# Kernel optimization log

Hardware: AMD Instinct MI355X
Metric: run time of the kernel (lower is better)

## Reference

```python
import jax, jax.numpy as jnp
import numpy as np

EPSILON = 0.1


def setup_inputs() -> dict:
    key = jax.random.key(0)
    ks = jax.random.split(key, 6)
    N, E, F_IN, F_OUT, NF = 50000, 800000, 256, 96, 3
    x = jax.random.normal(ks[0], (N, F_IN), dtype=jnp.float32)
    adj_vals = jax.random.uniform(ks[1], (E,), dtype=jnp.float32)
    d_scales = jax.random.uniform(ks[2], (NF, N), dtype=jnp.float32)
    # xavier-uniform-ish weights
    limit = np.sqrt(6.0 / (F_IN + F_OUT)).astype(np.float32)
    weights = jax.random.uniform(ks[3], (NF, F_IN, F_OUT), dtype=jnp.float32,
                                 minval=-limit, maxval=limit)
    bias = jnp.zeros((F_OUT,), dtype=jnp.float32)
    edge_index = jax.random.randint(ks[4], (2, E), 0, N, dtype=jnp.int32)
    return {"x": x, "adj_vals": adj_vals, "d_scales": d_scales,
            "weights": weights, "bias": bias, "edge_index": edge_index}


def reference(x, adj_vals, d_scales, weights, bias, edge_index):
    N = x.shape[0]
    row, col = edge_index[0], edge_index[1]

    # degree with self loops (add_remaining_self_loops adds 1 per node)
    deg = jax.ops.segment_sum(jnp.ones_like(adj_vals), row, num_segments=N) + 1.0
    eps_deg_inv = EPSILON / deg  # [N], diagonal of sparse_degree(..., epsilon)

    def spmm(t):  # symadj @ t via edge list
        return jax.ops.segment_sum(adj_vals[:, None] * t[col], row, num_segments=N)

    out = jnp.zeros((N, weights.shape[2]), dtype=x.dtype)
    n_filters = weights.shape[0]
    for ii in range(n_filters):
        sign = -1.0 if ii == 0 else 1.0  # Ad = symadj -/+ eps*diag(deg^-1)
        t = d_scales[ii][:, None] * (x @ weights[ii])          # D @ (x W)
        t = spmm(t) + sign * eps_deg_inv[:, None] * t          # Ad @ t
        t = d_scales[ii][:, None] * jax.nn.relu(t)             # D @ relu(t)
        out = out + t
    return out + bias
```

## Files before the change

### kernel.cpp

```cpp
#include <hip/hip_runtime.h>

#define EPSILON 0.1f
#define F_IN 256
#define F_OUT 96
#define NF 3
#define TCOLS 288
#define TSTRIDE 320
#define CAP 64
#define BLD 40
#define CLD 296
#define NCVT (TCOLS * F_IN / 4)

typedef __attribute__((ext_vector_type(8))) short bf8_t;
typedef __attribute__((ext_vector_type(4))) float f32x4;

__device__ inline ushort f2b(float f) {
    union { float f; unsigned u; } v; v.f = f;
    unsigned u = v.u;
    return (ushort)((u + 0x7FFFu + ((u >> 16) & 1u)) >> 16);
}
__device__ inline float blo(unsigned u) { return __uint_as_float(u << 16); }
__device__ inline float bhi(unsigned u) { return __uint_as_float(u & 0xffff0000u); }

__device__ inline bf8_t cvt8(float4 a, float4 b) {
    bf8_t r;
    r[0] = (short)f2b(a.x); r[1] = (short)f2b(a.y);
    r[2] = (short)f2b(a.z); r[3] = (short)f2b(a.w);
    r[4] = (short)f2b(b.x); r[5] = (short)f2b(b.y);
    r[6] = (short)f2b(b.z); r[7] = (short)f2b(b.w);
    return r;
}

__global__ __launch_bounds__(256) void setup_kernel(const float* __restrict__ w,
                                                    ushort* __restrict__ wt,
                                                    int* __restrict__ cnt, int N) {
    int tid = blockIdx.x * 256 + threadIdx.x;
    if (tid < NCVT) {
        int base = tid * 4;
        int gc = base >> 8;
        int k  = base & 255;
        int ii = gc / F_OUT;
        int c  = gc - ii * F_OUT;
        const float* wp = w + (size_t)ii * (F_IN * F_OUT) + (size_t)k * F_OUT + c;
        ushort4 o;
        o.x = f2b(wp[0 * F_OUT]);
        o.y = f2b(wp[1 * F_OUT]);
        o.z = f2b(wp[2 * F_OUT]);
        o.w = f2b(wp[3 * F_OUT]);
        *(ushort4*)(wt + base) = o;
    } else {
        int z = (tid - NCVT) * 4;
        if (z + 3 < N) {
            *(int4*)(cnt + z) = make_int4(0, 0, 0, 0);
        } else {
            for (int j = z; j < N && j >= 0; ++j) cnt[j] = 0;
        }
    }
}

__global__ __launch_bounds__(256) void scatter_kernel(const int* __restrict__ row,
                                                      const int* __restrict__ col,
                                                      const float* __restrict__ vals,
                                                      int* __restrict__ cnt,
                                                      int2* __restrict__ evs2, int E) {
    int i0 = (blockIdx.x * 256 + threadIdx.x) * 4;
    if (i0 + 3 < E) {
        int4   r4 = *(const int4*)(row + i0);
        int4   c4 = *(const int4*)(col + i0);
        float4 v4 = *(const float4*)(vals + i0);
        int k;
        k = atomicAdd(&cnt[r4.x], 1);
        if (k < CAP) evs2[(size_t)r4.x * CAP + k] = make_int2(c4.x, __float_as_int(v4.x));
        k = atomicAdd(&cnt[r4.y], 1);
        if (k < CAP) evs2[(size_t)r4.y * CAP + k] = make_int2(c4.y, __float_as_int(v4.y));
        k = atomicAdd(&cnt[r4.z], 1);
        if (k < CAP) evs2[(size_t)r4.z * CAP + k] = make_int2(c4.z, __float_as_int(v4.z));
        k = atomicAdd(&cnt[r4.w], 1);
        if (k < CAP) evs2[(size_t)r4.w * CAP + k] = make_int2(c4.w, __float_as_int(v4.w));
    } else {
        for (int i = i0; i < E; ++i) {
            int r = row[i];
            int k = atomicAdd(&cnt[r], 1);
            if (k < CAP) evs2[(size_t)r * CAP + k] = make_int2(col[i], __float_as_int(vals[i]));
        }
    }
}

__global__ __launch_bounds__(256) void gemm_mfma(const float* __restrict__ x,
                                                 const ushort* __restrict__ wt,
                                                 const float* __restrict__ dsc,
                                                 ushort* __restrict__ t, int N) {
    __shared__ ushort Bs[4 * 16 * CLD];

    int tid = threadIdx.x;
    int lane = tid & 63, wave = tid >> 6;
    int cl = lane & 15, quad = lane >> 4;
    int m0 = blockIdx.x * 64 + wave * 16;
    int mrow = m0 + cl;
    bool aok = (mrow < N);

    f32x4 acc[18];
    #pragma unroll
    for (int j = 0; j < 18; ++j) acc[j] = (f32x4){0.f, 0.f, 0.f, 0.f};

    const float* xp = x + (size_t)mrow * F_IN + quad * 8;
    const float4 fz = make_float4(0.f, 0.f, 0.f, 0.f);
    float4 pa0 = aok ? *(const float4*)(xp)     : fz;
    float4 pa1 = aok ? *(const float4*)(xp + 4) : fz;

    for (int ks = 0; ks < F_IN; ks += 32) {
        __syncthreads();
        #pragma unroll
        for (int it = 0; it < 5; ++it) {
            int idx = tid + it * 256;
            if (idx < TCOLS * 4) {
                int gc = idx >> 2, kc = (idx & 3) * 8;
                *(uint4*)(Bs + gc * BLD + kc) =
                    *(const uint4*)(wt + (size_t)gc * F_IN + ks + kc);
            }
        }
        __syncthreads();
        bf8_t a = cvt8(pa0, pa1);
        int kn = ks + 32;
        if (kn < F_IN) {
            pa0 = aok ? *(const float4*)(xp + kn)     : fz;
            pa1 = aok ? *(const float4*)(xp + kn + 4) : fz;
        }
        const ushort* bb = Bs + cl * BLD + quad * 8;
        #pragma unroll
        for (int j = 0; j < 18; ++j) {
            bf8_t b = *(const bf8_t*)(bb + j * 16 * BLD);
            acc[j] = __builtin_amdgcn_mfma_f32_16x16x32_bf16(a, b, acc[j], 0, 0, 0);
        }
    }

    __syncthreads();
    ushort* Cw = Bs + wave * (16 * CLD);
    float dscv[3][4];
    #pragma unroll
    for (int ii = 0; ii < 3; ++ii)
        #pragma unroll
        for (int r = 0; r < 4; ++r) {
            int rowg = m0 + quad * 4 + r;
            dscv[ii][r] = (rowg < N) ? dsc[(size_t)ii * N + rowg] : 0.f;
        }
    #pragma unroll
    for (int j = 0; j < 18; ++j) {
        int ii = j / 6;
        #pragma unroll
        for (int r = 0; r < 4; ++r)
            Cw[(quad * 4 + r) * CLD + j * 16 + cl] = f2b(dscv[ii][r] * acc[j][r]);
    }
    #pragma unroll
    for (int it = 0; it < 9; ++it) {
        int idx = lane + it * 64;
        int r = idx / 36, ch = idx - r * 36;
        int grow = m0 + r;
        if (grow < N)
            *(uint4*)(t + (size_t)grow * TSTRIDE + ch * 8) =
                *(const uint4*)&Cw[r * CLD + ch * 8];
    }
}

__device__ inline void acc8(float* acc, uint4 a, float v) {
    acc[0] = fmaf(v, blo(a.x), acc[0]); acc[1] = fmaf(v, bhi(a.x), acc[1]);
    acc[2] = fmaf(v, blo(a.y), acc[2]); acc[3] = fmaf(v, bhi(a.y), acc[3]);
    acc[4] = fmaf(v, blo(a.z), acc[4]); acc[5] = fmaf(v, bhi(a.z), acc[5]);
    acc[6] = fmaf(v, blo(a.w), acc[6]); acc[7] = fmaf(v, bhi(a.w), acc[7]);
}

__global__ __launch_bounds__(256) void spmm_kernel(const ushort* __restrict__ t,
                                                   const int2* __restrict__ evs2,
                                                   const int* __restrict__ cnt,
                                                   const float* __restrict__ dsc,
                                                   const float* __restrict__ bias,
                                                   float* __restrict__ out, int N) {
    int lane = threadIdx.x & 63;
    int wave = threadIdx.x >> 6;
    int n = blockIdx.x * 4 + wave;
    if (n >= N) return;

    int deg = cnt[n];
    int mm = (deg < CAP) ? deg : CAP;
    int s = n * CAP, e = s + mm;
    int coff = (lane < 40) ? lane * 8 : 0;

    float acc[8];
    #pragma unroll
    for (int j = 0; j < 8; ++j) acc[j] = 0.f;

    for (int base = s; base < e; base += 64) {
        int idx = base + lane;
        int2 q = make_int2(0, 0);
        if (idx < e) q = evs2[idx];
        int m = min(64, e - base);
        int j = 0;
        for (; j + 3 < m; j += 4) {
            int c0 = __shfl(q.x, j, 64);
            int c1 = __shfl(q.x, j + 1, 64);
            int c2 = __shfl(q.x, j + 2, 64);
            int c3 = __shfl(q.x, j + 3, 64);
            float v0 = __int_as_float(__shfl(q.y, j, 64));
            float v1 = __int_as_float(__shfl(q.y, j + 1, 64));
            float v2 = __int_as_float(__shfl(q.y, j + 2, 64));
            float v3 = __int_as_float(__shfl(q.y, j + 3, 64));
            uint4 a0 = *(const uint4*)(t + (size_t)c0 * TSTRIDE + coff);
            uint4 a1 = *(const uint4*)(t + (size_t)c1 * TSTRIDE + coff);
            uint4 a2 = *(const uint4*)(t + (size_t)c2 * TSTRIDE + coff);
            uint4 a3 = *(const uint4*)(t + (size_t)c3 * TSTRIDE + coff);
            acc8(acc, a0, v0);
            acc8(acc, a1, v1);
            acc8(acc, a2, v2);
            acc8(acc, a3, v3);
        }
        for (; j < m; ++j) {
            int c = __shfl(q.x, j, 64);
            float v = __int_as_float(__shfl(q.y, j, 64));
            uint4 a = *(const uint4*)(t + (size_t)c * TSTRIDE + coff);
            acc8(acc, a, v);
        }
    }

    float sign = (lane < 12) ? -1.f : 1.f;
    float epsdi = EPSILON / (float)(deg + 1);
    int ii = lane / 12;
    float dscv = (lane < 36) ? dsc[(size_t)ii * N + n] : 0.f;
    uint4 sv = *(const uint4*)(t + (size_t)n * TSTRIDE + coff);
    float se = sign * epsdi;
    float val[8];
    {
        unsigned u;
        u = sv.x; val[0] = fmaf(se, blo(u), acc[0]); val[1] = fmaf(se, bhi(u), acc[1]);
        u = sv.y; val[2] = fmaf(se, blo(u), acc[2]); val[3] = fmaf(se, bhi(u), acc[3]);
        u = sv.z; val[4] = fmaf(se, blo(u), acc[4]); val[5] = fmaf(se, bhi(u), acc[5]);
        u = sv.w; val[6] = fmaf(se, blo(u), acc[6]); val[7] = fmaf(se, bhi(u), acc[7]);
    }
    #pragma unroll
    for (int j = 0; j < 8; ++j) val[j] = fmaxf(val[j], 0.f) * dscv;

    float res[8];
    #pragma unroll
    for (int j = 0; j < 8; ++j) {
        float r1 = __shfl(val[j], lane + 12, 64);
        float r2 = __shfl(val[j], lane + 24, 64);
        res[j] = val[j] + r1 + r2;
    }
    if (lane < 12) {
        float4 b0 = *(const float4*)(bias + lane * 8);
        float4 b1 = *(const float4*)(bias + lane * 8 + 4);
        float4 o0 = make_float4(res[0] + b0.x, res[1] + b0.y, res[2] + b0.z, res[3] + b0.w);
        float4 o1 = make_float4(res[4] + b1.x, res[5] + b1.y, res[6] + b1.z, res[7] + b1.w);
        *(float4*)(out + (size_t)n * F_OUT + lane * 8) = o0;
        *(float4*)(out + (size_t)n * F_OUT + lane * 8 + 4) = o1;
    }
}

extern "C" void kernel_launch(void* const* d_in, const int* in_sizes, int n_in,
                              void* d_out, int out_size, void* d_ws, size_t ws_size,
                              hipStream_t stream) {
    const float* x    = (const float*)d_in[0];
    const float* adj  = (const float*)d_in[1];
    const float* dsc  = (const float*)d_in[2];
    const float* w    = (const float*)d_in[3];
    const float* bias = (const float*)d_in[4];
    const int*   ei   = (const int*)d_in[5];

    int E = in_sizes[1];
    int N = in_sizes[0] / F_IN;
    const int* row = ei;
    const int* col = ei + E;
    float* out = (float*)d_out;

    char* p = (char*)d_ws;
    auto take = [&](size_t bytes) {
        char* r = p;
        p += (bytes + 255) & ~(size_t)255;
        return r;
    };
    int*    cnt  = (int*)take((size_t)N * 4);
    int2*   evs2 = (int2*)take((size_t)N * CAP * 8);
    ushort* wt   = (ushort*)take((size_t)TCOLS * F_IN * 2);
    ushort* t    = (ushort*)take(((size_t)N * TSTRIDE + 256) * 2);

    int nzero = (N + 3) / 4;
    setup_kernel<<<(NCVT + nzero + 255) / 256, 256, 0, stream>>>(w, wt, cnt, N);
    scatter_kernel<<<(E / 4 + 255) / 256, 256, 0, stream>>>(row, col, adj, cnt, evs2, E);
    gemm_mfma<<<(N + 63) / 64, 256, 0, stream>>>(x, wt, dsc, t, N);
    spmm_kernel<<<(N + 3) / 4, 256, 0, stream>>>(t, evs2, cnt, dsc, bias, out, N);
}
```

Before: 270.4 us.

## Split GEMM over three column blocks and preload full-K weight tile into LDS

The GEMM grid is split by output column block (one filter per block), so each block computes 96 columns instead of 288. The whole 96x256 bf16 weight slice is loaded into LDS once in an MFMA-fragment-friendly layout, which removes the per-k-step syncthreads and reload. Accumulator registers drop from 18 to 6 tiles, which should improve occupancy. In exchange, each x row is now read and converted three times across blocks.

```diff
diff --git a/kernel.cpp b/kernel.cpp
--- a/kernel.cpp
+++ b/kernel.cpp
@@ -7,8 +7,8 @@
 #define TCOLS 288
 #define TSTRIDE 320
 #define CAP 64
-#define BLD 40
-#define CLD 296
+#define BN 96
+#define CW 104
 #define NCVT (TCOLS * F_IN / 4)
 
 typedef __attribute__((ext_vector_type(8))) short bf8_t;
@@ -90,52 +90,57 @@
                                                  const ushort* __restrict__ wt,
                                                  const float* __restrict__ dsc,
                                                  ushort* __restrict__ t, int N) {
-    __shared__ ushort Bs[4 * 16 * CLD];
+    __shared__ ushort Bs[BN * F_IN];
 
     int tid = threadIdx.x;
     int lane = tid & 63, wave = tid >> 6;
     int cl = lane & 15, quad = lane >> 4;
-    int m0 = blockIdx.x * 64 + wave * 16;
+    int mb = blockIdx.x / 3, cb = blockIdx.x - mb * 3;
+    int gc0 = cb * BN;
+    int m0 = mb * 64 + wave * 16;
     int mrow = m0 + cl;
     bool aok = (mrow < N);
 
-    f32x4 acc[18];
-    #pragma unroll
-    for (int j = 0; j < 18; ++j) acc[j] = (f32x4){0.f, 0.f, 0.f, 0.f};
+    #pragma unroll
+    for (int i = 0; i < 12; ++i) {
+        int F = tid + i * 256;
+        int rem = F & 63;
+        int q = rem >> 4, c = rem & 15;
+        int ksj = F >> 6;
+        int ks = ksj / 6, j = ksj - ks * 6;
+        int gc = gc0 + j * 16 + c;
+        *(uint4*)(Bs + (size_t)F * 8) =
+            *(const uint4*)(wt + (size_t)gc * F_IN + ks * 32 + q * 8);
+    }
+
+    f32x4 acc[6];
+    #pragma unroll
+    for (int j = 0; j < 6; ++j) acc[j] = (f32x4){0.f, 0.f, 0.f, 0.f};
 
     const float* xp = x + (size_t)mrow * F_IN + quad * 8;
     const float4 fz = make_float4(0.f, 0.f, 0.f, 0.f);
     float4 pa0 = aok ? *(const float4*)(xp)     : fz;
     float4 pa1 = aok ? *(const float4*)(xp + 4) : fz;
 
-    for (int ks = 0; ks < F_IN; ks += 32) {
-        __syncthreads();
+    __syncthreads();
+
+    #pragma unroll
+    for (int ks = 0; ks < 8; ++ks) {
+        bf8_t a = cvt8(pa0, pa1);
+        if (ks < 7) {
+            pa0 = aok ? *(const float4*)(xp + (ks + 1) * 32)     : fz;
+            pa1 = aok ? *(const float4*)(xp + (ks + 1) * 32 + 4) : fz;
+        }
+        const ushort* bb = Bs + ((size_t)(ks * 6) * 64 + lane) * 8;
         #pragma unroll
-        for (int it = 0; it < 5; ++it) {
-            int idx = tid + it * 256;
-            if (idx < TCOLS * 4) {
-                int gc = idx >> 2, kc = (idx & 3) * 8;
-                *(uint4*)(Bs + gc * BLD + kc) =
-                    *(const uint4*)(wt + (size_t)gc * F_IN + ks + kc);
-            }
-        }
-        __syncthreads();
-        bf8_t a = cvt8(pa0, pa1);
-        int kn = ks + 32;
-        if (kn < F_IN) {
-            pa0 = aok ? *(const float4*)(xp + kn)     : fz;
-            pa1 = aok ? *(const float4*)(xp + kn + 4) : fz;
-        }
-        const ushort* bb = Bs + cl * BLD + quad * 8;
-        #pragma unroll
-        for (int j = 0; j < 18; ++j) {
-            bf8_t b = *(const bf8_t*)(bb + j * 16 * BLD);
+        for (int j = 0; j < 6; ++j) {
+            bf8_t b = *(const bf8_t*)(bb + j * 64 * 8);
             acc[j] = __builtin_amdgcn_mfma_f32_16x16x32_bf16(a, b, acc[j], 0, 0, 0);
         }
     }
 
     __syncthreads();
-    ushort* Cw = Bs + wave * (16 * CLD);
+    ushort* Cw = Bs + wave * (16 * CW);
     float dscv[3][4];
     #pragma unroll
     for (int ii = 0; ii < 3; ++ii)
@@ -145,20 +150,20 @@
             dscv[ii][r] = (rowg < N) ? dsc[(size_t)ii * N + rowg] : 0.f;
         }
     #pragma unroll
-    for (int j = 0; j < 18; ++j) {
-        int ii = j / 6;
+    for (int j = 0; j < 6; ++j) {
+        int ii = (gc0 + j * 16) / F_OUT;
         #pragma unroll
         for (int r = 0; r < 4; ++r)
-            Cw[(quad * 4 + r) * CLD + j * 16 + cl] = f2b(dscv[ii][r] * acc[j][r]);
-    }
-    #pragma unroll
-    for (int it = 0; it < 9; ++it) {
+            Cw[(quad * 4 + r) * CW + j * 16 + cl] = f2b(dscv[ii][r] * acc[j][r]);
+    }
+    #pragma unroll
+    for (int it = 0; it < 3; ++it) {
         int idx = lane + it * 64;
-        int r = idx / 36, ch = idx - r * 36;
+        int r = idx / 12, ch = idx - r * 12;
         int grow = m0 + r;
         if (grow < N)
-            *(uint4*)(t + (size_t)grow * TSTRIDE + ch * 8) =
-                *(const uint4*)&Cw[r * CLD + ch * 8];
+            *(uint4*)(t + (size_t)grow * TSTRIDE + gc0 + ch * 8) =
+                *(const uint4*)&Cw[r * CW + ch * 8];
     }
 }
 
@@ -285,6 +290,6 @@
     int nzero = (N + 3) / 4;
     setup_kernel<<<(NCVT + nzero + 255) / 256, 256, 0, stream>>>(w, wt, cnt, N);
     scatter_kernel<<<(E / 4 + 255) / 256, 256, 0, stream>>>(row, col, adj, cnt, evs2, E);
-    gemm_mfma<<<(N + 63) / 64, 256, 0, stream>>>(x, wt, dsc, t, N);
+    gemm_mfma<<<3 * ((N + 63) / 64), 256, 0, stream>>>(x, wt, dsc, t, N);
     spmm_kernel<<<(N + 3) / 4, 256, 0, stream>>>(t, evs2, cnt, dsc, bias, out, N);
 }
```

After: 294.2 us. 1.09x slower.
